# Kernel tuning notes

Measured on AMD Instinct MI355X. Metric: run time of the kernel, lower is better.

Reference implementation:

```python
import jax, jax.numpy as jnp
import numpy as np

N_NODES = 100000
N_EDGES = 1000000
NHID = 128
N_CLASSES = 5000


def setup_inputs() -> dict:
    key = jax.random.key(0)
    ks = jax.random.split(key, 8)
    feature = jax.random.normal(ks[0], (N_NODES, NHID), dtype=jnp.float32)
    # Linear weights stored as [in, out] so forward is x @ W + b
    W1 = jax.random.normal(ks[1], (2 * NHID, NHID), dtype=jnp.float32) * (1.0 / np.sqrt(2 * NHID))
    b1 = jnp.zeros((NHID,), dtype=jnp.float32)
    alpha = jnp.full((NHID,), 0.25, dtype=jnp.float32)  # PReLU per-channel init
    W2 = jax.random.normal(ks[2], (NHID, 2), dtype=jnp.float32) * (1.0 / np.sqrt(NHID))
    b2 = jnp.zeros((2,), dtype=jnp.float32)
    row = jax.random.randint(ks[3], (N_EDGES,), 0, N_NODES, dtype=jnp.int64)
    col = jax.random.randint(ks[4], (N_EDGES,), 0, N_NODES, dtype=jnp.int64)
    label = jax.random.randint(ks[5], (N_NODES,), 0, N_CLASSES, dtype=jnp.int64)
    return {"feature": feature, "W1": W1, "b1": b1, "alpha": alpha,
            "W2": W2, "b2": b2, "row": row, "col": col, "label": label}


def reference(feature, W1, b1, alpha, W2, b2, row, col, label):
    # per-edge label: 1 if endpoints share a cluster label
    y = (label[row] == label[col]).astype(jnp.int32)  # [E]
    # edge gather + concat: [E, 2*nhid]
    x = jnp.concatenate([feature[row], feature[col]], axis=1)
    h = x @ W1 + b1                                   # [E, nhid]
    h = jnp.where(h >= 0, h, alpha * h)               # PReLU, per-channel alpha
    logits = h @ W2 + b2                              # [E, 2]
    logp = jax.nn.log_softmax(logits, axis=-1)
    # mean cross-entropy over edges
    loss = -jnp.mean(jnp.take_along_axis(logp, y[:, None], axis=1))
    return loss
```

## Files before the change

kernel.cpp:

```cpp
#include <hip/hip_runtime.h>
#include <hip/hip_bf16.h>

typedef __bf16 bf16_t;
typedef bf16_t bf16x8 __attribute__((ext_vector_type(8)));
typedef float floatx4 __attribute__((ext_vector_type(4)));
typedef float floatx2 __attribute__((ext_vector_type(2)));

#define N_NODES 100000
#define N_EDGES 1000000


__global__ __launch_bounds__(256) void k_prep(const float* __restrict__ W1,
                                              const float* __restrict__ b1,
                                              const float* __restrict__ alpha,
                                              const float* __restrict__ W2,
                                              const float* __restrict__ b2,
                                              bf16_t* __restrict__ WT,
                                              float* __restrict__ wabsp,
                                              float* __restrict__ w1g,
                                              float* __restrict__ constg,
                                              float* __restrict__ out) {
    const int t = threadIdx.x;
    if (blockIdx.x < 128) {
        int i = blockIdx.x * 256 + t;
        int n = i >> 7, k = i & 127;
        float v = (n < 128) ? W1[k * 128 + n] : W1[(k + 128) * 128 + (n - 128)];
        WT[i] = (bf16_t)v;
        return;
    }
    __shared__ float w1L[128];
    if (t < 128) {
        float wd = W2[2 * t + 1] - W2[2 * t];
        float al = alpha[t];
        float w1v = wd * (1.f + al) * 0.5f;
        w1L[t] = w1v;
        w1g[t] = w1v;
        int col = (t & 64) + (t & 3) * 16 + ((t >> 2) & 15);
        float wdc = W2[2 * col + 1] - W2[2 * col];
        wabsp[t] = wdc * (1.f - alpha[col]) * 0.5f;
    }
    __syncthreads();
    if (t < 64) {
        float c = fmaf(w1L[t], b1[t], w1L[t + 64] * b1[t + 64]);
#pragma unroll
        for (int m = 32; m >= 1; m >>= 1) c += __shfl_xor(c, m, 64);
        if (t == 0) { *constg = c + (b2[1] - b2[0]); out[0] = 0.f; }
    }
}

__global__ __launch_bounds__(256) void k_gemm(const float* __restrict__ F,
                                              const bf16_t* __restrict__ WT,
                                              const float* __restrict__ b1,
                                              const float* __restrict__ w1g,
                                              const int* __restrict__ label,
                                              unsigned char* __restrict__ PQ8,
                                              float* __restrict__ aux_g) {
    __shared__ bf16x8 Bs[2048];
    __shared__ float sP[4][16];
    const int t = threadIdx.x;
    const int h = blockIdx.x & 1;
    const int m0 = (blockIdx.x >> 1) * 32;

    const bf16x8* WT8 = (const bf16x8*)WT + (size_t)h * 2048;
#pragma unroll
    for (int j = 0; j < 8; ++j) {
        int chunk = j * 256 + t;
        int c = chunk >> 4, cc = chunk & 15;
        Bs[c * 16 + (cc ^ (c & 15))] = WT8[chunk];
    }

    const int w = t >> 6, lane = t & 63;
    const int l15 = lane & 15, quad = lane >> 4;
    const int rw = w >> 1, wq = w & 1;

    const int arow = m0 + rw * 16 + l15;
    const float4* Ar = (const float4*)(F + (size_t)arow * 128 + quad * 8);
    float4 fa[4], fb[4];
#pragma unroll
    for (int s = 0; s < 4; ++s) { fa[s] = Ar[s * 8]; fb[s] = Ar[s * 8 + 1]; }

    float w1v[4], bv[4];
#pragma unroll
    for (int nt = 0; nt < 4; ++nt) {
        int c = wq * 64 + nt * 16 + l15;
        w1v[nt] = w1g[c];
        bv[nt] = (h == 0) ? b1[c] : 0.f;
    }

    bf16x8 Af[4];
#pragma unroll
    for (int s = 0; s < 4; ++s) {
        bf16x8 v;
        v[0] = (bf16_t)fa[s].x; v[1] = (bf16_t)fa[s].y;
        v[2] = (bf16_t)fa[s].z; v[3] = (bf16_t)fa[s].w;
        v[4] = (bf16_t)fb[s].x; v[5] = (bf16_t)fb[s].y;
        v[6] = (bf16_t)fb[s].z; v[7] = (bf16_t)fb[s].w;
        Af[s] = v;
    }
    __syncthreads();

    floatx4 acc[4] = {};
#pragma unroll
    for (int s = 0; s < 4; ++s) {
        bf16x8 Bf[4];
#pragma unroll
        for (int nt = 0; nt < 4; ++nt) {
            int c = wq * 64 + nt * 16 + l15;
            Bf[nt] = Bs[c * 16 + ((s * 4 + quad) ^ (c & 15))];
        }
#pragma unroll
        for (int nt = 0; nt < 4; ++nt)
            acc[nt] = __builtin_amdgcn_mfma_f32_16x16x32_bf16(Af[s], Bf[nt], acc[nt], 0, 0, 0);
    }

    float pr[4];
#pragma unroll
    for (int r = 0; r < 4; ++r) {
        float sv = 0.f;
#pragma unroll
        for (int nt = 0; nt < 4; ++nt) sv = fmaf(w1v[nt], acc[nt][r], sv);
#pragma unroll
        for (int m = 8; m >= 1; m >>= 1) sv += __shfl_xor(sv, m, 64);
        pr[r] = sv;
    }
    if (l15 == 0) {
#pragma unroll
        for (int r = 0; r < 4; ++r) sP[w][quad * 4 + r] = pr[r];
    }

#pragma unroll
    for (int r = 0; r < 4; ++r) {
        int g = m0 + rw * 16 + quad * 4 + r;
        unsigned int pk = 0;
        pk = __builtin_amdgcn_cvt_pk_fp8_f32(acc[0][r] + bv[0], acc[1][r] + bv[1], pk, false);
        pk = __builtin_amdgcn_cvt_pk_fp8_f32(acc[2][r] + bv[2], acc[3][r] + bv[3], pk, true);
        *(unsigned int*)(PQ8 + (size_t)g * 256 + h * 128 + wq * 64 + l15 * 4) = pk;
    }

    __syncthreads();
    if (t < 32) {
        int rw2 = t >> 4, ri = t & 15;
        float v = sP[rw2 * 2][ri] + sP[rw2 * 2 + 1][ri];
        int g = m0 + rw2 * 16 + ri;
        if (h == 0) {
            aux_g[(size_t)g * 4 + 0] = v;
            ((int*)aux_g)[(size_t)g * 4 + 2] = label[g];
        } else {
            aux_g[(size_t)g * 4 + 1] = v;
        }
    }
}

__global__ __launch_bounds__(256) void k_edge_loss(const unsigned char* __restrict__ PQ8,
                                                   const float4* __restrict__ aux,
                                                   const float* __restrict__ wabsp,
                                                   const float* __restrict__ constg,
                                                   const int* __restrict__ row,
                                                   const int* __restrict__ col,
                                                   float* __restrict__ out) {
    const int lg = threadIdx.x & 15;
    const int group = (blockIdx.x * blockDim.x + threadIdx.x) >> 4;
    const int ng = (gridDim.x * blockDim.x) >> 4;
    const int ch = lg * 8;

    float wabs[8];
#pragma unroll
    for (int j = 0; j < 8; ++j) wabs[j] = wabsp[ch + j];
    const float CB = *constg;

    float acc = 0.f;
    for (int e = group; e < N_EDGES; e += 8 * ng) {
        int r[8], c[8];
#pragma unroll
        for (int k = 0; k < 8; ++k) {
            int ee = e + k * ng;
            int es = (ee < N_EDGES) ? ee : e;
            r[k] = row[es]; c[k] = col[es];
        }
        uint2 p[8], q[8];
#pragma unroll
        for (int k = 0; k < 8; ++k) {
            p[k] = *(const uint2*)(PQ8 + (size_t)r[k] * 256 + ch);
            q[k] = *(const uint2*)(PQ8 + (size_t)c[k] * 256 + 128 + ch);
        }
        int ee2 = e + (lg & 7) * ng;
        int es2 = (ee2 < N_EDGES) ? ee2 : e;
        const int* ibase = (lg < 8) ? row : col;
        float4 a = aux[ibase[es2]];

        float sab[8] = {0.f, 0.f, 0.f, 0.f, 0.f, 0.f, 0.f, 0.f};
#pragma unroll
        for (int k = 0; k < 8; ++k) {
            floatx2 p01 = __builtin_amdgcn_cvt_pk_f32_fp8((int)p[k].x, false);
            floatx2 p23 = __builtin_amdgcn_cvt_pk_f32_fp8((int)p[k].x, true);
            floatx2 p45 = __builtin_amdgcn_cvt_pk_f32_fp8((int)p[k].y, false);
            floatx2 p67 = __builtin_amdgcn_cvt_pk_f32_fp8((int)p[k].y, true);
            floatx2 q01 = __builtin_amdgcn_cvt_pk_f32_fp8((int)q[k].x, false);
            floatx2 q23 = __builtin_amdgcn_cvt_pk_f32_fp8((int)q[k].x, true);
            floatx2 q45 = __builtin_amdgcn_cvt_pk_f32_fp8((int)q[k].y, false);
            floatx2 q67 = __builtin_amdgcn_cvt_pk_f32_fp8((int)q[k].y, true);
            floatx2 h01 = p01 + q01;
            floatx2 h23 = p23 + q23;
            floatx2 h45 = p45 + q45;
            floatx2 h67 = p67 + q67;
            float s = sab[k];
            s = fmaf(fabsf(h01[0]), wabs[0], s);
            s = fmaf(fabsf(h01[1]), wabs[1], s);
            s = fmaf(fabsf(h23[0]), wabs[2], s);
            s = fmaf(fabsf(h23[1]), wabs[3], s);
            s = fmaf(fabsf(h45[0]), wabs[4], s);
            s = fmaf(fabsf(h45[1]), wabs[5], s);
            s = fmaf(fabsf(h67[0]), wabs[6], s);
            s = fmaf(fabsf(h67[1]), wabs[7], s);
            sab[k] = s;
        }
#pragma unroll
        for (int m = 8; m >= 1; m >>= 1) {
#pragma unroll
            for (int k = 0; k < 8; ++k) sab[k] += __shfl_xor(sab[k], m, 16);
        }
        float s2o = __shfl(a.y, (lg + 8) & 15, 16);
        float lzc = __shfl(a.z, (lg + 8) & 15, 16);
        float mysab = sab[0];
#pragma unroll
        for (int k = 1; k < 8; ++k) mysab = (lg == k) ? sab[k] : mysab;
        float D = a.x + s2o + CB + mysab;
        float sgn = (__float_as_int(a.z) == __float_as_int(lzc)) ? -D : D;
        float loss = fmaxf(sgn, 0.f) + __logf(1.f + __expf(-fabsf(sgn)));
        bool vld = (lg < 8) && (e + lg * ng < N_EDGES);
        acc += vld ? loss : 0.f;
    }
#pragma unroll
    for (int m = 32; m >= 1; m >>= 1) acc += __shfl_xor(acc, m, 64);
    __shared__ float sdata[4];
    int lane = threadIdx.x & 63;
    int wv = threadIdx.x >> 6;
    if (lane == 0) sdata[wv] = acc;
    __syncthreads();
    if (threadIdx.x == 0) {
        float s = (sdata[0] + sdata[1]) + (sdata[2] + sdata[3]);
        atomicAdd(out, s * (1.f / (float)N_EDGES));
    }
}

extern "C" void kernel_launch(void* const* d_in, const int* in_sizes, int n_in,
                              void* d_out, int out_size, void* d_ws, size_t ws_size,
                              hipStream_t stream) {
    const float* feature = (const float*)d_in[0];
    const float* W1      = (const float*)d_in[1];
    const float* b1      = (const float*)d_in[2];
    const float* alpha   = (const float*)d_in[3];
    const float* W2      = (const float*)d_in[4];
    const float* b2      = (const float*)d_in[5];
    const int*   row     = (const int*)d_in[6];
    const int*   col     = (const int*)d_in[7];
    const int*   label   = (const int*)d_in[8];
    float* out = (float*)d_out;

    char* ws = (char*)d_ws;
    unsigned char* PQ8 = (unsigned char*)(ws);
    float* aux   = (float*)(ws + 25600000);
    bf16_t* WT   = (bf16_t*)(ws + 27200000);
    float* wabsp = (float*)(ws + 27265536);
    float* w1g   = (float*)(ws + 27266048);
    float* constg= (float*)(ws + 27266560);

    k_prep<<<129, 256, 0, stream>>>(W1, b1, alpha, W2, b2, WT, wabsp, w1g,
                                    constg, out);
    k_gemm<<<6250, 256, 0, stream>>>(feature, WT, b1, w1g, label, PQ8, aux);
    k_edge_loss<<<4096, 256, 0, stream>>>(PQ8, (const float4*)aux, wabsp, constg,
                                          row, col, out);
}
```

Before: 198.0 us.

## Quantize per-node projections to FP4 codes and compute both halves per block

```diff
diff --git a/kernel.cpp b/kernel.cpp
--- a/kernel.cpp
+++ b/kernel.cpp
@@ -48,43 +48,50 @@
     }
 }
 
+__device__ inline unsigned fp4_code(float x) {
+    float a = fabsf(x);
+    unsigned code = (unsigned)(a > 0.25f) + (a > 0.75f) + (a > 1.25f) + (a > 1.75f)
+                  + (a > 2.5f) + (a > 3.5f) + (a > 5.0f);
+    return code | (x < 0.f ? 8u : 0u);
+}
+
 __global__ __launch_bounds__(256) void k_gemm(const float* __restrict__ F,
                                               const bf16_t* __restrict__ WT,
                                               const float* __restrict__ b1,
                                               const float* __restrict__ w1g,
                                               const int* __restrict__ label,
-                                              unsigned char* __restrict__ PQ8,
-                                              float* __restrict__ aux_g) {
+                                              unsigned char* __restrict__ PQ4,
+                                              float4* __restrict__ aux_g) {
     __shared__ bf16x8 Bs[2048];
-    __shared__ float sP[4][16];
+    __shared__ float sP1[4][16];
+    __shared__ float sP2[4][16];
     const int t = threadIdx.x;
-    const int h = blockIdx.x & 1;
-    const int m0 = (blockIdx.x >> 1) * 32;
-
-    const bf16x8* WT8 = (const bf16x8*)WT + (size_t)h * 2048;
+    const int m0 = blockIdx.x * 32;
+
+    const int w = t >> 6, lane = t & 63;
+    const int l15 = lane & 15, quad = lane >> 4;
+    const int rw = w >> 1, wq = w & 1;
+
+    const int arow = m0 + rw * 16 + l15;
+    const float4* Ar = (const float4*)(F + (size_t)arow * 128 + quad * 8);
+    float4 fa[4], fb[4];
+#pragma unroll
+    for (int s = 0; s < 4; ++s) { fa[s] = Ar[s * 8]; fb[s] = Ar[s * 8 + 1]; }
+
+    float w1v[4], bv[4];
+#pragma unroll
+    for (int nt = 0; nt < 4; ++nt) {
+        int c = wq * 64 + nt * 16 + l15;
+        w1v[nt] = w1g[c];
+        bv[nt] = b1[c];
+    }
+
+    const bf16x8* WT8 = (const bf16x8*)WT;
 #pragma unroll
     for (int j = 0; j < 8; ++j) {
         int chunk = j * 256 + t;
         int c = chunk >> 4, cc = chunk & 15;
         Bs[c * 16 + (cc ^ (c & 15))] = WT8[chunk];
-    }
-
-    const int w = t >> 6, lane = t & 63;
-    const int l15 = lane & 15, quad = lane >> 4;
-    const int rw = w >> 1, wq = w & 1;
-
-    const int arow = m0 + rw * 16 + l15;
-    const float4* Ar = (const float4*)(F + (size_t)arow * 128 + quad * 8);
-    float4 fa[4], fb[4];
-#pragma unroll
-    for (int s = 0; s < 4; ++s) { fa[s] = Ar[s * 8]; fb[s] = Ar[s * 8 + 1]; }
-
-    float w1v[4], bv[4];
-#pragma unroll
-    for (int nt = 0; nt < 4; ++nt) {
-        int c = wq * 64 + nt * 16 + l15;
-        w1v[nt] = w1g[c];
-        bv[nt] = (h == 0) ? b1[c] : 0.f;
     }
 
     bf16x8 Af[4];
@@ -99,59 +106,79 @@
     }
     __syncthreads();
 
-    floatx4 acc[4] = {};
-#pragma unroll
-    for (int s = 0; s < 4; ++s) {
-        bf16x8 Bf[4];
-#pragma unroll
-        for (int nt = 0; nt < 4; ++nt) {
-            int c = wq * 64 + nt * 16 + l15;
-            Bf[nt] = Bs[c * 16 + ((s * 4 + quad) ^ (c & 15))];
-        }
-#pragma unroll
-        for (int nt = 0; nt < 4; ++nt)
-            acc[nt] = __builtin_amdgcn_mfma_f32_16x16x32_bf16(Af[s], Bf[nt], acc[nt], 0, 0, 0);
-    }
-
-    float pr[4];
-#pragma unroll
-    for (int r = 0; r < 4; ++r) {
-        float sv = 0.f;
-#pragma unroll
-        for (int nt = 0; nt < 4; ++nt) sv = fmaf(w1v[nt], acc[nt][r], sv);
-#pragma unroll
-        for (int m = 8; m >= 1; m >>= 1) sv += __shfl_xor(sv, m, 64);
-        pr[r] = sv;
-    }
-    if (l15 == 0) {
-#pragma unroll
-        for (int r = 0; r < 4; ++r) sP[w][quad * 4 + r] = pr[r];
-    }
-
-#pragma unroll
-    for (int r = 0; r < 4; ++r) {
-        int g = m0 + rw * 16 + quad * 4 + r;
-        unsigned int pk = 0;
-        pk = __builtin_amdgcn_cvt_pk_fp8_f32(acc[0][r] + bv[0], acc[1][r] + bv[1], pk, false);
-        pk = __builtin_amdgcn_cvt_pk_fp8_f32(acc[2][r] + bv[2], acc[3][r] + bv[3], pk, true);
-        *(unsigned int*)(PQ8 + (size_t)g * 256 + h * 128 + wq * 64 + l15 * 4) = pk;
+#pragma unroll
+    for (int h = 0; h < 2; ++h) {
+        floatx4 acc[4] = {};
+#pragma unroll
+        for (int s = 0; s < 4; ++s) {
+            bf16x8 Bf[4];
+#pragma unroll
+            for (int nt = 0; nt < 4; ++nt) {
+                int c = wq * 64 + nt * 16 + l15;
+                Bf[nt] = Bs[c * 16 + ((s * 4 + quad) ^ (c & 15))];
+            }
+#pragma unroll
+            for (int nt = 0; nt < 4; ++nt)
+                acc[nt] = __builtin_amdgcn_mfma_f32_16x16x32_bf16(Af[s], Bf[nt], acc[nt], 0, 0, 0);
+        }
+
+#pragma unroll
+        for (int r = 0; r < 4; ++r) {
+            float sv = 0.f;
+#pragma unroll
+            for (int nt = 0; nt < 4; ++nt) sv = fmaf(w1v[nt], acc[nt][r], sv);
+#pragma unroll
+            for (int m = 8; m >= 1; m >>= 1) sv += __shfl_xor(sv, m, 64);
+            if (l15 == 0) {
+                if (h == 0) sP1[w][quad * 4 + r] = sv;
+                else        sP2[w][quad * 4 + r] = sv;
+            }
+        }
+
+#pragma unroll
+        for (int r = 0; r < 4; ++r) {
+            int g = m0 + rw * 16 + quad * 4 + r;
+            float v0 = acc[0][r], v1 = acc[1][r], v2 = acc[2][r], v3 = acc[3][r];
+            if (h == 0) { v0 += bv[0]; v1 += bv[1]; v2 += bv[2]; v3 += bv[3]; }
+            unsigned pk = fp4_code(v0) | (fp4_code(v1) << 4)
+                        | (fp4_code(v2) << 8) | (fp4_code(v3) << 12);
+            *(unsigned short*)(PQ4 + (size_t)g * 128 + h * 64 + wq * 32 + l15 * 2) =
+                (unsigned short)pk;
+        }
+
+        if (h == 0) {
+            __syncthreads();
+#pragma unroll
+            for (int j = 0; j < 8; ++j) {
+                int chunk = j * 256 + t;
+                int c = chunk >> 4, cc = chunk & 15;
+                Bs[c * 16 + (cc ^ (c & 15))] = WT8[2048 + chunk];
+            }
+            __syncthreads();
+        }
     }
 
     __syncthreads();
     if (t < 32) {
         int rw2 = t >> 4, ri = t & 15;
-        float v = sP[rw2 * 2][ri] + sP[rw2 * 2 + 1][ri];
+        float s1 = sP1[rw2 * 2][ri] + sP1[rw2 * 2 + 1][ri];
+        float s2 = sP2[rw2 * 2][ri] + sP2[rw2 * 2 + 1][ri];
         int g = m0 + rw2 * 16 + ri;
-        if (h == 0) {
-            aux_g[(size_t)g * 4 + 0] = v;
-            ((int*)aux_g)[(size_t)g * 4 + 2] = label[g];
-        } else {
-            aux_g[(size_t)g * 4 + 1] = v;
-        }
-    }
-}
-
-__global__ __launch_bounds__(256) void k_edge_loss(const unsigned char* __restrict__ PQ8,
+        float4 av = {s1, s2, __int_as_float(label[g]), 0.f};
+        aux_g[g] = av;
+    }
+}
+
+__device__ inline void fp4_decode(unsigned d, unsigned& pe, unsigned& po) {
+    unsigned ne = d & 0x0F0F0F0Fu;
+    unsigned no = (d >> 4) & 0x0F0F0F0Fu;
+    pe = __builtin_amdgcn_perm(0x4C484440u, 0x3C383000u, ne & 0x07070707u)
+       | ((ne & 0x08080808u) << 4);
+    po = __builtin_amdgcn_perm(0x4C484440u, 0x3C383000u, no & 0x07070707u)
+       | ((no & 0x08080808u) << 4);
+}
+
+__global__ __launch_bounds__(256) void k_edge_loss(const unsigned char* __restrict__ PQ4,
                                                    const float4* __restrict__ aux,
                                                    const float* __restrict__ wabsp,
                                                    const float* __restrict__ constg,
@@ -161,11 +188,11 @@
     const int lg = threadIdx.x & 15;
     const int group = (blockIdx.x * blockDim.x + threadIdx.x) >> 4;
     const int ng = (gridDim.x * blockDim.x) >> 4;
-    const int ch = lg * 8;
 
     float wabs[8];
-#pragma unroll
-    for (int j = 0; j < 8; ++j) wabs[j] = wabsp[ch + j];
+    const float* wb = wabsp + lg * 8;
+    wabs[0] = wb[0]; wabs[1] = wb[2]; wabs[2] = wb[4]; wabs[3] = wb[6];
+    wabs[4] = wb[1]; wabs[5] = wb[3]; wabs[6] = wb[5]; wabs[7] = wb[7];
     const float CB = *constg;
 
     float acc = 0.f;
@@ -177,11 +204,11 @@
             int es = (ee < N_EDGES) ? ee : e;
             r[k] = row[es]; c[k] = col[es];
         }
-        uint2 p[8], q[8];
+        unsigned p[8], q[8];
 #pragma unroll
         for (int k = 0; k < 8; ++k) {
-            p[k] = *(const uint2*)(PQ8 + (size_t)r[k] * 256 + ch);
-            q[k] = *(const uint2*)(PQ8 + (size_t)c[k] * 256 + 128 + ch);
+            p[k] = *(const unsigned*)(PQ4 + (size_t)r[k] * 128 + lg * 4);
+            q[k] = *(const unsigned*)(PQ4 + (size_t)c[k] * 128 + 64 + lg * 4);
         }
         int ee2 = e + (lg & 7) * ng;
         int es2 = (ee2 < N_EDGES) ? ee2 : e;
@@ -191,27 +218,26 @@
         float sab[8] = {0.f, 0.f, 0.f, 0.f, 0.f, 0.f, 0.f, 0.f};
 #pragma unroll
         for (int k = 0; k < 8; ++k) {
-            floatx2 p01 = __builtin_amdgcn_cvt_pk_f32_fp8((int)p[k].x, false);
-            floatx2 p23 = __builtin_amdgcn_cvt_pk_f32_fp8((int)p[k].x, true);
-            floatx2 p45 = __builtin_amdgcn_cvt_pk_f32_fp8((int)p[k].y, false);
-            floatx2 p67 = __builtin_amdgcn_cvt_pk_f32_fp8((int)p[k].y, true);
-            floatx2 q01 = __builtin_amdgcn_cvt_pk_f32_fp8((int)q[k].x, false);
-            floatx2 q23 = __builtin_amdgcn_cvt_pk_f32_fp8((int)q[k].x, true);
-            floatx2 q45 = __builtin_amdgcn_cvt_pk_f32_fp8((int)q[k].y, false);
-            floatx2 q67 = __builtin_amdgcn_cvt_pk_f32_fp8((int)q[k].y, true);
-            floatx2 h01 = p01 + q01;
-            floatx2 h23 = p23 + q23;
-            floatx2 h45 = p45 + q45;
-            floatx2 h67 = p67 + q67;
+            unsigned pe, po, qe, qo;
+            fp4_decode(p[k], pe, po);
+            fp4_decode(q[k], qe, qo);
+            floatx2 he0 = __builtin_amdgcn_cvt_pk_f32_fp8((int)pe, false)
+                        + __builtin_amdgcn_cvt_pk_f32_fp8((int)qe, false);
+            floatx2 he1 = __builtin_amdgcn_cvt_pk_f32_fp8((int)pe, true)
+                        + __builtin_amdgcn_cvt_pk_f32_fp8((int)qe, true);
+            floatx2 ho0 = __builtin_amdgcn_cvt_pk_f32_fp8((int)po, false)
+                        + __builtin_amdgcn_cvt_pk_f32_fp8((int)qo, false);
+            floatx2 ho1 = __builtin_amdgcn_cvt_pk_f32_fp8((int)po, true)
+                        + __builtin_amdgcn_cvt_pk_f32_fp8((int)qo, true);
             float s = sab[k];
-            s = fmaf(fabsf(h01[0]), wabs[0], s);
-            s = fmaf(fabsf(h01[1]), wabs[1], s);
-            s = fmaf(fabsf(h23[0]), wabs[2], s);
-            s = fmaf(fabsf(h23[1]), wabs[3], s);
-            s = fmaf(fabsf(h45[0]), wabs[4], s);
-            s = fmaf(fabsf(h45[1]), wabs[5], s);
-            s = fmaf(fabsf(h67[0]), wabs[6], s);
-            s = fmaf(fabsf(h67[1]), wabs[7], s);
+            s = fmaf(fabsf(he0[0]), wabs[0], s);
+            s = fmaf(fabsf(he0[1]), wabs[1], s);
+            s = fmaf(fabsf(he1[0]), wabs[2], s);
+            s = fmaf(fabsf(he1[1]), wabs[3], s);
+            s = fmaf(fabsf(ho0[0]), wabs[4], s);
+            s = fmaf(fabsf(ho0[1]), wabs[5], s);
+            s = fmaf(fabsf(ho1[0]), wabs[6], s);
+            s = fmaf(fabsf(ho1[1]), wabs[7], s);
             sab[k] = s;
         }
 #pragma unroll
@@ -258,16 +284,17 @@
     float* out = (float*)d_out;
 
     char* ws = (char*)d_ws;
-    unsigned char* PQ8 = (unsigned char*)(ws);
-    float* aux   = (float*)(ws + 25600000);
-    bf16_t* WT   = (bf16_t*)(ws + 27200000);
-    float* wabsp = (float*)(ws + 27265536);
-    float* w1g   = (float*)(ws + 27266048);
-    float* constg= (float*)(ws + 27266560);
+    unsigned char* PQ4 = (unsigned char*)(ws);
+    float* aux   = (float*)(ws + 12800000);
+    bf16_t* WT   = (bf16_t*)(ws + 14400000);
+    float* wabsp = (float*)(ws + 14465536);
+    float* w1g   = (float*)(ws + 14466048);
+    float* constg= (float*)(ws + 14466560);
 
     k_prep<<<129, 256, 0, stream>>>(W1, b1, alpha, W2, b2, WT, wabsp, w1g,
                                     constg, out);
-    k_gemm<<<6250, 256, 0, stream>>>(feature, WT, b1, w1g, label, PQ8, aux);
-    k_edge_loss<<<4096, 256, 0, stream>>>(PQ8, (const float4*)aux, wabsp, constg,
+    k_gemm<<<3125, 256, 0, stream>>>(feature, WT, b1, w1g, label, PQ4,
+                                     (float4*)aux);
+    k_edge_loss<<<4096, 256, 0, stream>>>(PQ4, (const float4*)aux, wabsp, constg,
                                           row, col, out);
 }
```

Result: faster. 192.2 us (-2.9%).
